# Optimization experiments

Measured on AMD Instinct MI355X. Metric: run time of the kernel, lower is better.

The kernel has to match this reference:

```python
import jax, jax.numpy as jnp
import numpy as np
from jax import lax

# Config matching init_kwargs
H, W = 64, 64
DIM = 160
HEADS = 5
KD = DIM // HEADS            # key_dim = head_dim = 32 (attn_ratio=1 -> d == key_dim)
WS = 14                       # window size -> n = 196 tokens per window
HIDDEN = int(DIM * 4.0)
EPS = 1e-5


def _make_bias_idxs(ws):
    pts = [(i, j) for i in range(ws) for j in range(ws)]
    offs, idxs = {}, []
    for p1 in pts:
        for p2 in pts:
            o = (abs(p1[0] - p2[0]), abs(p1[1] - p2[1]))
            if o not in offs:
                offs[o] = len(offs)
            idxs.append(offs[o])
    n = len(pts)
    return np.asarray(idxs, np.int32).reshape(n, n), len(offs)


def setup_inputs() -> dict:
    key = jax.random.key(0)
    ks = jax.random.split(key, 10)
    bias_idxs_np, n_off = _make_bias_idxs(WS)  # [196,196], 196 unique offsets
    s = 0.02
    return {
        "x": jax.random.normal(ks[0], (16, H * W, DIM), jnp.float32),
        "ln1_g": jnp.ones((DIM,), jnp.float32),
        "ln1_b": jnp.zeros((DIM,), jnp.float32),
        "qkv_w": jax.random.normal(ks[1], (3 * KD * HEADS, DIM), jnp.float32) * s,
        "qkv_b": jnp.zeros((3 * KD * HEADS,), jnp.float32),
        "proj_w": jax.random.normal(ks[2], (DIM, KD * HEADS), jnp.float32) * s,
        "proj_b": jnp.zeros((DIM,), jnp.float32),
        "attn_biases": jax.random.normal(ks[3], (HEADS, n_off), jnp.float32) * s,
        "conv_w": jax.random.normal(ks[4], (DIM, 1, 3, 3), jnp.float32) * s,  # depthwise OIHW
        "bn_g": jnp.ones((DIM,), jnp.float32),
        "bn_b": jnp.zeros((DIM,), jnp.float32),
        "ln2_g": jnp.ones((DIM,), jnp.float32),
        "ln2_b": jnp.zeros((DIM,), jnp.float32),
        "fc1_w": jax.random.normal(ks[5], (HIDDEN, DIM), jnp.float32) * s,
        "fc1_b": jnp.zeros((HIDDEN,), jnp.float32),
        "fc2_w": jax.random.normal(ks[6], (DIM, HIDDEN), jnp.float32) * s,
        "fc2_b": jnp.zeros((DIM,), jnp.float32),
        "bias_idxs": jnp.asarray(bias_idxs_np),
    }


def _layernorm(x, g, b):
    m = jnp.mean(x, -1, keepdims=True)
    v = jnp.mean(jnp.square(x - m), -1, keepdims=True)
    return (x - m) * lax.rsqrt(v + EPS) * g + b


def reference(x, ln1_g, ln1_b, qkv_w, qkv_b, proj_w, proj_b, attn_biases,
              conv_w, bn_g, bn_b, ln2_g, ln2_b, fc1_w, fc1_b, fc2_w, fc2_b,
              bias_idxs):
    b, l, c = x.shape
    res = x
    # ---- window partition (64 -> pad 70 -> 5x5 windows of 14x14 = 196 tokens)
    pad_b = (WS - H % WS) % WS
    pad_r = (WS - W % WS) % WS
    xg = x.reshape(b, H, W, c)
    xg = jnp.pad(xg, ((0, 0), (0, pad_b), (0, pad_r), (0, 0)))
    ph, pw = H + pad_b, W + pad_r
    nh, nw = ph // WS, pw // WS
    n = WS * WS
    xw = xg.reshape(b, nh, WS, nw, WS, c).transpose(0, 1, 3, 2, 4, 5).reshape(b * nh * nw, n, c)
    # ---- attention with gathered relative-position bias
    xn = _layernorm(xw, ln1_g, ln1_b)
    qkv = (xn @ qkv_w.T + qkv_b).reshape(xw.shape[0], n, HEADS, 3 * KD)
    q, k, v = qkv[..., :KD], qkv[..., KD:2 * KD], qkv[..., 2 * KD:]
    bias = attn_biases[:, bias_idxs]  # [HEADS, n, n]
    scores = jnp.einsum('bnhd,bmhd->bhnm', q, k) * (KD ** -0.5) + bias
    a = jax.nn.softmax(scores, axis=-1)
    out = jnp.einsum('bhnm,bmhd->bnhd', a, v).reshape(xw.shape[0], n, HEADS * KD)
    xw = out @ proj_w.T + proj_b
    # ---- window merge + unpad
    xg = xw.reshape(b, nh, nw, WS, WS, c).transpose(0, 1, 3, 2, 4, 5).reshape(b, ph, pw, c)
    xg = xg[:, :H, :W]
    x = res + xg.reshape(b, l, c)
    # ---- depthwise 3x3 conv + BN (eval: running_mean=0, running_var=1)
    xc = x.transpose(0, 2, 1).reshape(b, c, H, W)
    y = lax.conv_general_dilated(xc, conv_w, (1, 1), [(1, 1), (1, 1)],
                                 dimension_numbers=('NCHW', 'OIHW', 'NCHW'),
                                 feature_group_count=c)
    y = y * (bn_g * lax.rsqrt(jnp.float32(1.0 + EPS)))[None, :, None, None] + bn_b[None, :, None, None]
    x = y.reshape(b, c, l).transpose(0, 2, 1)
    # ---- MLP with pre-LN and exact GELU
    xn = _layernorm(x, ln2_g, ln2_b)
    h = jax.nn.gelu(xn @ fc1_w.T + fc1_b, approximate=False)
    m = h @ fc2_w.T + fc2_b
    return x + m
```

## Files before the change

kernel.cpp:

```cpp
#include <hip/hip_runtime.h>
#include <hip/hip_bf16.h>
#include <math.h>

typedef unsigned short ushort;
typedef __attribute__((ext_vector_type(4))) float f32x4;
typedef __attribute__((ext_vector_type(8))) short s16x8;
typedef __attribute__((ext_vector_type(4))) short s16x4;
typedef __attribute__((ext_vector_type(4))) ushort u16x4;

#define H_    64
#define W_    64
#define DIM   160
#define HEADS 5
#define KD    32
#define WS    14
#define NTOK  196
#define NWIN  400
#define HIDDEN 640
#define EPS   1e-5f
#define NROW  (NWIN*NTOK)
#define BATCH 16
#define L_    (H_*W_)
#define MROW  (BATCH*L_)
#define CS    0.25507875861f
#define GSTRIPS 4

#if __has_builtin(__builtin_amdgcn_exp2f)
#define EXP2(x) __builtin_amdgcn_exp2f(x)
#else
#define EXP2(x) exp2f(x)
#endif

__device__ __forceinline__ ushort f2bfbits(float f) {
    unsigned u = __float_as_uint(f);
    unsigned r = (u + 0x7fffu + ((u >> 16) & 1u)) >> 16;
    return (ushort)r;
}

__global__ __launch_bounds__(256) void pre_kernel(
    const float* __restrict__ qkv_w, const float* __restrict__ proj_w,
    const float* __restrict__ fc1_w, const float* __restrict__ fc2_w,
    const float* __restrict__ conv_w, const float* __restrict__ bn_g,
    const float* __restrict__ abias, const int* __restrict__ bidx,
    ushort* __restrict__ wb, float* __restrict__ cwT,
    float* __restrict__ biasP, int n_off)
{
    const int gid = blockIdx.x * 256 + threadIdx.x;
    if (gid < 19200) {
        float4 v = ((const float4*)qkv_w)[gid];
        u16x4 o = { f2bfbits(v.x), f2bfbits(v.y), f2bfbits(v.z), f2bfbits(v.w) };
        *(u16x4*)(wb + gid * 4) = o;
    } else if (gid < 25600) {
        const int i = gid - 19200;
        float4 v = ((const float4*)proj_w)[i];
        u16x4 o = { f2bfbits(v.x), f2bfbits(v.y), f2bfbits(v.z), f2bfbits(v.w) };
        *(u16x4*)(wb + 76800 + i * 4) = o;
    } else if (gid < 38400) {
        const int idx = gid - 25600;
        const int l = idx & 63, rest = idx >> 6;
        const int jj = rest % 5, ht = rest / 5;
        const float* src = fc1_w + (size_t)(ht * 16 + (l & 15)) * 160
                         + jj * 32 + (l >> 4) * 8;
        const float4 v0 = *(const float4*)src;
        const float4 v1 = *(const float4*)(src + 4);
        u16x4 o0 = { f2bfbits(v0.x), f2bfbits(v0.y), f2bfbits(v0.z), f2bfbits(v0.w) };
        u16x4 o1 = { f2bfbits(v1.x), f2bfbits(v1.y), f2bfbits(v1.z), f2bfbits(v1.w) };
        *(u16x4*)(wb + 102400 + idx * 8)     = o0;
        *(u16x4*)(wb + 102400 + idx * 8 + 4) = o1;
    } else if (gid < 51200) {
        const int idx = gid - 38400;
        const int l = idx & 63, f = idx >> 6;
        const int dt = f % 10, u = f / 10;
        const float* base = fc2_w + (size_t)(dt * 16 + (l & 15)) * HIDDEN
                          + u * 32 + 4 * (l >> 4);
        const float4 v0 = *(const float4*)base;
        const float4 v1 = *(const float4*)(base + 16);
        u16x4 o0 = { f2bfbits(v0.x), f2bfbits(v0.y), f2bfbits(v0.z), f2bfbits(v0.w) };
        u16x4 o1 = { f2bfbits(v1.x), f2bfbits(v1.y), f2bfbits(v1.z), f2bfbits(v1.w) };
        *(u16x4*)(wb + 204800 + idx * 8)     = o0;
        *(u16x4*)(wb + 204800 + idx * 8 + 4) = o1;
    } else if (gid < 51560) {
        const int i = gid - 51200;
        const int t = i / 40, c4 = (i % 40) * 4;
#pragma unroll
        for (int j = 0; j < 4; ++j) {
            const int c = c4 + j;
            cwT[t * DIM + c] = conv_w[c * 9 + t] * bn_g[c] * rsqrtf(1.0f + EPS);
        }
    } else if (gid < 267880) {
        const int idx = gid - 51560;
        const int ln = idx & 255, f = idx >> 8;
        const int h = f / 169, rem = f % 169;
        const int qt = rem / 13, kt = rem % 13;
        int q = qt * 16 + (ln & 15); if (q > NTOK - 1) q = NTOK - 1;
        const int k0 = kt * 16 + (ln >> 4) * 4;
        float4 o;
        float* ov = (float*)&o;
#pragma unroll
        for (int r = 0; r < 4; ++r) {
            const int k = k0 + r;
            ov[r] = (k < NTOK)
                ? abias[h * n_off + bidx[q * NTOK + k]] * 1.4426950408889634f
                : 0.f;
        }
        *(float4*)(biasP + (size_t)idx * 4) = o;
    }
}

__global__ __launch_bounds__(256) void ln1_win_kernel(
    const float* __restrict__ x, const float* __restrict__ g,
    const float* __restrict__ b, ushort* __restrict__ xn)
{
    const int row = blockIdx.x * 4 + (threadIdx.x >> 6);
    const int win = row / NTOK, tok = row % NTOK;
    const int bb = win / 25, wr = (win % 25) / 5, wc = win % 5;
    const int gh = wr * WS + tok / WS, gw = wc * WS + tok % WS;
    const bool valid = (gh < H_) && (gw < W_);
    const float* xrow = x + ((size_t)bb * L_ + (size_t)gh * W_ + gw) * DIM;
    const int lane = threadIdx.x & 63;
    float v0 = 0.f, v1 = 0.f, v2 = 0.f;
    if (valid) {
        v0 = xrow[lane];
        v1 = xrow[lane + 64];
        if (lane < 32) v2 = xrow[lane + 128];
    }
    float s  = v0 + v1 + v2;
    float sq = v0 * v0 + v1 * v1 + v2 * v2;
#pragma unroll
    for (int off = 32; off; off >>= 1) { s += __shfl_xor(s, off); sq += __shfl_xor(sq, off); }
    const float mean = s * (1.0f / DIM);
    const float var  = sq * (1.0f / DIM) - mean * mean;
    const float rs   = rsqrtf(var + EPS);
    ushort* orow = xn + (size_t)row * DIM;
    orow[lane]      = f2bfbits((v0 - mean) * rs * g[lane]      + b[lane]);
    orow[lane + 64] = f2bfbits((v1 - mean) * rs * g[lane + 64] + b[lane + 64]);
    if (lane < 32) orow[lane + 128] = f2bfbits((v2 - mean) * rs * g[lane + 128] + b[lane + 128]);
}

template <int EPI>
__global__ __launch_bounds__(512) void gemm_mfma(
    const ushort* __restrict__ A, const ushort* __restrict__ Wb,
    const float* __restrict__ bias, void* __restrict__ Cv,
    const float* __restrict__ extra, int M, int N)
{
    __shared__ ushort Bs[160][164];
    const int tid = threadIdx.x;
    const int wv = tid >> 6, ln = tid & 63;
    const int g = ln >> 4, l15 = ln & 15;
    const int wvm = wv & 3, wvn = wv >> 2;
    const int n0 = blockIdx.y * 160;
    const int strip0 = blockIdx.x * GSTRIPS;

    for (int e = tid; e < 160 * 20; e += 512) {
        const int row = e / 20, part = e % 20;
        *(int4*)&Bs[row][part * 8] =
            *(const int4*)(Wb + (size_t)(n0 + row) * 160 + part * 8);
    }

    s16x8 a[2][5];
    {
        const int m0 = strip0 * 128;
#pragma unroll
        for (int mt = 0; mt < 2; ++mt) {
            int am = m0 + wvm * 32 + mt * 16 + l15; if (am >= M) am = M - 1;
            const ushort* ap = A + (size_t)am * 160 + g * 8;
#pragma unroll
            for (int s = 0; s < 5; ++s) a[mt][s] = *(const s16x8*)(ap + s * 32);
        }
    }
    __syncthreads();

    for (int s = 0; s < GSTRIPS; ++s) {
        const int m0 = (strip0 + s) * 128;
        if (m0 >= M) break;

        f32x4 acc[2][5] = {};
#pragma unroll
        for (int j = 0; j < 5; ++j) {
#pragma unroll
            for (int nt = 0; nt < 5; ++nt) {
                const s16x8 bf = *(const s16x8*)&Bs[wvn * 80 + nt * 16 + l15][j * 32 + g * 8];
                acc[0][nt] = __builtin_amdgcn_mfma_f32_16x16x32_bf16(bf, a[0][j], acc[0][nt], 0, 0, 0);
                acc[1][nt] = __builtin_amdgcn_mfma_f32_16x16x32_bf16(bf, a[1][j], acc[1][nt], 0, 0, 0);
            }
        }

        if (s + 1 < GSTRIPS) {
            const int mn = (strip0 + s + 1) * 128;
#pragma unroll
            for (int mt = 0; mt < 2; ++mt) {
                int am = mn + wvm * 32 + mt * 16 + l15; if (am >= M) am = M - 1;
                const ushort* ap = A + (size_t)am * 160 + g * 8;
#pragma unroll
                for (int jj = 0; jj < 5; ++jj) a[mt][jj] = *(const s16x8*)(ap + jj * 32);
            }
        }

#pragma unroll
        for (int mt = 0; mt < 2; ++mt) {
            const int m = m0 + wvm * 32 + mt * 16 + l15;
            if (m >= M) continue;
            if (EPI == 0) {
                ushort* orow = (ushort*)Cv + (size_t)m * N;
#pragma unroll
                for (int nt = 0; nt < 5; ++nt) {
                    const int n = n0 + wvn * 80 + nt * 16 + g * 4;
                    const float4 bn = *(const float4*)&bias[n];
                    const float sc = ((n % 96) < 32) ? CS : 1.0f;
                    u16x4 o = { f2bfbits((acc[mt][nt][0] + bn.x) * sc),
                                f2bfbits((acc[mt][nt][1] + bn.y) * sc),
                                f2bfbits((acc[mt][nt][2] + bn.z) * sc),
                                f2bfbits((acc[mt][nt][3] + bn.w) * sc) };
                    *(u16x4*)(orow + n) = o;
                }
            } else {
                const int win = m / NTOK, tok = m % NTOK;
                const int bb = win / 25, wr = (win % 25) / 5, wc = win % 5;
                const int gh = wr * WS + tok / WS, gw = wc * WS + tok % WS;
                if (gh < H_ && gw < W_) {
                    const size_t rowoff = ((size_t)bb * L_ + (size_t)gh * W_ + gw) * DIM;
                    float* orow = (float*)Cv + rowoff;
                    const float* erow = extra + rowoff;
#pragma unroll
                    for (int nt = 0; nt < 5; ++nt) {
                        const int n = n0 + wvn * 80 + nt * 16 + g * 4;
                        const float4 bn = *(const float4*)&bias[n];
                        const float4 res = *(const float4*)&erow[n];
                        float4 o4 = { res.x + acc[mt][nt][0] + bn.x,
                                      res.y + acc[mt][nt][1] + bn.y,
                                      res.z + acc[mt][nt][2] + bn.z,
                                      res.w + acc[mt][nt][3] + bn.w };
                        *(float4*)&orow[n] = o4;
                    }
                }
            }
        }
    }
}

__global__ __launch_bounds__(256, 3) void mlp_fused(
    float* xo, const ushort* __restrict__ w1p, const ushort* __restrict__ w2p,
    const float* __restrict__ fc1_b, const float* __restrict__ fc2_b,
    const float* __restrict__ lng, const float* __restrict__ lnb)
{
    __shared__ ushort W1s[10240];
    __shared__ ushort W2s[10240];
    const int tid = threadIdx.x;
    const int wv = tid >> 6, ln = tid & 63;
    const int g = ln >> 4, l15 = ln & 15;
    const int row0 = blockIdx.x * 64 + wv * 16;

    const float* xp = xo + (size_t)(row0 + l15) * DIM + g * 8;
    float4 va[10];
    float vsum = 0.f, vsq = 0.f;
#pragma unroll
    for (int s = 0; s < 5; ++s) {
        const float4 p0 = *(const float4*)(xp + s * 32);
        const float4 p1 = *(const float4*)(xp + s * 32 + 4);
        va[s * 2] = p0; va[s * 2 + 1] = p1;
        vsum += (p0.x + p0.y) + (p0.z + p0.w) + (p1.x + p1.y) + (p1.z + p1.w);
        vsq  += (p0.x*p0.x + p0.y*p0.y) + (p0.z*p0.z + p0.w*p0.w)
              + (p1.x*p1.x + p1.y*p1.y) + (p1.z*p1.z + p1.w*p1.w);
    }
    vsum += __shfl_xor(vsum, 16); vsum += __shfl_xor(vsum, 32);
    vsq  += __shfl_xor(vsq, 16);  vsq  += __shfl_xor(vsq, 32);
    const float mean = vsum * (1.0f / DIM);
    const float rs = rsqrtf(vsq * (1.0f / DIM) - mean * mean + EPS);
    s16x8 a1[5];
#pragma unroll
    for (int s = 0; s < 5; ++s) {
        const float4 g0 = *(const float4*)(lng + s * 32 + g * 8);
        const float4 g1 = *(const float4*)(lng + s * 32 + g * 8 + 4);
        const float4 bb0 = *(const float4*)(lnb + s * 32 + g * 8);
        const float4 bb1 = *(const float4*)(lnb + s * 32 + g * 8 + 4);
        const float4 p0 = va[s * 2], p1 = va[s * 2 + 1];
        ushort o[8];
        o[0] = f2bfbits((p0.x - mean) * rs * g0.x + bb0.x);
        o[1] = f2bfbits((p0.y - mean) * rs * g0.y + bb0.y);
        o[2] = f2bfbits((p0.z - mean) * rs * g0.z + bb0.z);
        o[3] = f2bfbits((p0.w - mean) * rs * g0.w + bb0.w);
        o[4] = f2bfbits((p1.x - mean) * rs * g1.x + bb1.x);
        o[5] = f2bfbits((p1.y - mean) * rs * g1.y + bb1.y);
        o[6] = f2bfbits((p1.z - mean) * rs * g1.z + bb1.z);
        o[7] = f2bfbits((p1.w - mean) * rs * g1.w + bb1.w);
        a1[s] = *(const s16x8*)o;
    }

    f32x4 oacc[10] = {};
    for (int c = 0; c < 10; ++c) {
        if (c) __syncthreads();
        const ushort* s1 = w1p + c * 10240;
        const ushort* s2 = w2p + c * 10240;
        for (int e = tid; e < 1280; e += 256) {
            *(int4*)&W1s[e * 8] = *(const int4*)(s1 + e * 8);
            *(int4*)&W2s[e * 8] = *(const int4*)(s2 + e * 8);
        }
        __syncthreads();

#pragma unroll
        for (int p = 0; p < 2; ++p) {
            f32x4 h0 = {0.f,0.f,0.f,0.f}, h1 = {0.f,0.f,0.f,0.f};
#pragma unroll
            for (int jj = 0; jj < 5; ++jj) {
                const s16x8 wfe = *(const s16x8*)&W1s[(((p * 2) * 5 + jj) * 64 + ln) * 8];
                const s16x8 wfo = *(const s16x8*)&W1s[(((p * 2 + 1) * 5 + jj) * 64 + ln) * 8];
                h0 = __builtin_amdgcn_mfma_f32_16x16x32_bf16(wfe, a1[jj], h0, 0, 0, 0);
                h1 = __builtin_amdgcn_mfma_f32_16x16x32_bf16(wfo, a1[jj], h1, 0, 0, 0);
            }
            const int hb0 = c * 64 + p * 32 + g * 4;
            const float4 hbe = *(const float4*)(fc1_b + hb0);
            const float4 hbo = *(const float4*)(fc1_b + hb0 + 16);
            const float hbev[4] = { hbe.x, hbe.y, hbe.z, hbe.w };
            const float hbov[4] = { hbo.x, hbo.y, hbo.z, hbo.w };
            ushort pk[8];
#pragma unroll
            for (int r = 0; r < 4; ++r) {
                float v = h0[r] + hbev[r];
                float t = EXP2(-2.302259756f * fmaf(0.044715f * v * v, v, v));
                pk[r] = f2bfbits(v * __builtin_amdgcn_rcpf(1.0f + t));
                v = h1[r] + hbov[r];
                t = EXP2(-2.302259756f * fmaf(0.044715f * v * v, v, v));
                pk[4 + r] = f2bfbits(v * __builtin_amdgcn_rcpf(1.0f + t));
            }
            const s16x8 P = *(const s16x8*)pk;
#pragma unroll
            for (int dt = 0; dt < 10; ++dt) {
                const s16x8 w2f = *(const s16x8*)&W2s[((p * 10 + dt) * 64 + ln) * 8];
                oacc[dt] = __builtin_amdgcn_mfma_f32_16x16x32_bf16(P, w2f, oacc[dt], 0, 0, 0);
            }
        }
    }

#pragma unroll
    for (int dt = 0; dt < 10; ++dt) {
        const float bn = fc2_b[dt * 16 + l15];
#pragma unroll
        for (int r = 0; r < 4; ++r) {
            const size_t off = (size_t)(row0 + g * 4 + r) * DIM + dt * 16 + l15;
            xo[off] += oacc[dt][r] + bn;
        }
    }
}

__global__ __launch_bounds__(256) void attn_mfma_kernel(
    const ushort* __restrict__ qkv, const float* __restrict__ biasP,
    ushort* __restrict__ out)
{
    __shared__ ushort Ks[208][40];
    __shared__ ushort VT[32][212];
    const int win = blockIdx.x / HEADS;
    const int h   = blockIdx.x % HEADS;
    const int tid = threadIdx.x;
    const size_t base = (size_t)win * NTOK;
    const ushort* qbase = qkv + base * 480 + h * 96;

    for (int e = tid; e < 208 * 4; e += 256) {
        const int row = e >> 2, part = e & 3;
        const int gr = row < NTOK ? row : NTOK - 1;
        *(int4*)&Ks[row][part * 8] = *(const int4*)(qbase + (size_t)gr * 480 + 32 + part * 8);
    }
    for (int e = tid; e < NTOK * 4; e += 256) {
        const int key = e >> 2, part = e & 3;
        int4 p = *(const int4*)(qbase + (size_t)key * 480 + 64 + part * 8);
        const ushort* u = (const ushort*)&p;
#pragma unroll
        for (int j = 0; j < 8; ++j) VT[part * 8 + j][key] = u[j];
    }
    for (int e = tid; e < 12 * 32; e += 256) VT[e & 31][NTOK + (e >> 5)] = 0;
    __syncthreads();

    const int wv = tid >> 6, ln = tid & 63, g = ln >> 4, l15 = ln & 15;

    for (int qt = wv; qt < 13; qt += 4) {
        const int qr = qt * 16 + l15;
        const int qc = qr < NTOK ? qr : NTOK - 1;
        const s16x8 qf = *(const s16x8*)(qbase + (size_t)qc * 480 + g * 8);
        const float* bq = biasP + ((size_t)(h * 13 + qt) * 13) * 1024;

        f32x4 S[13];
#pragma unroll
        for (int kt = 0; kt < 13; ++kt)
            S[kt] = *(const f32x4*)(bq + kt * 1024 + ln * 4);
#pragma unroll
        for (int kt = 0; kt < 13; ++kt) {
            const s16x8 kf = *(const s16x8*)&Ks[kt * 16 + l15][g * 8];
            S[kt] = __builtin_amdgcn_mfma_f32_16x16x32_bf16(kf, qf, S[kt], 0, 0, 0);
        }
        float mx = -1e30f;
#pragma unroll
        for (int kt = 0; kt < 13; ++kt) {
#pragma unroll
            for (int r = 0; r < 4; ++r) {
                if (kt == 12) {
                    const int key = 192 + g * 4 + r;
                    if (key >= NTOK) S[kt][r] = -1e30f;
                }
                mx = fmaxf(mx, S[kt][r]);
            }
        }
        mx = fmaxf(mx, __shfl_xor(mx, 16));
        mx = fmaxf(mx, __shfl_xor(mx, 32));

        float sum = 0.f;
        s16x4 P[13];
#pragma unroll
        for (int kt = 0; kt < 13; ++kt) {
            const float p0 = EXP2(S[kt][0] - mx);
            const float p1 = EXP2(S[kt][1] - mx);
            const float p2 = EXP2(S[kt][2] - mx);
            const float p3 = EXP2(S[kt][3] - mx);
            sum += (p0 + p1) + (p2 + p3);
            P[kt] = (s16x4){ (short)f2bfbits(p0), (short)f2bfbits(p1),
                             (short)f2bfbits(p2), (short)f2bfbits(p3) };
        }
        sum += __shfl_xor(sum, 16);
        sum += __shfl_xor(sum, 32);

        f32x4 o0 = {0.f,0.f,0.f,0.f}, o1 = {0.f,0.f,0.f,0.f};
#pragma unroll
        for (int kt = 0; kt < 13; ++kt) {
            const s16x4 vf0 = *(const s16x4*)&VT[l15][kt * 16 + g * 4];
            const s16x4 vf1 = *(const s16x4*)&VT[16 + l15][kt * 16 + g * 4];
            o0 = __builtin_amdgcn_mfma_f32_16x16x16bf16_1k(vf0, P[kt], o0, 0, 0, 0);
            o1 = __builtin_amdgcn_mfma_f32_16x16x16bf16_1k(vf1, P[kt], o1, 0, 0, 0);
        }
        if (qr < NTOK) {
            const float inv = 1.0f / sum;
            ushort* op = out + (base + qr) * DIM + h * KD;
            u16x4 w0 = { f2bfbits(o0[0] * inv), f2bfbits(o0[1] * inv),
                         f2bfbits(o0[2] * inv), f2bfbits(o0[3] * inv) };
            u16x4 w1 = { f2bfbits(o1[0] * inv), f2bfbits(o1[1] * inv),
                         f2bfbits(o1[2] * inv), f2bfbits(o1[3] * inv) };
            *(u16x4*)(op + g * 4)      = w0;
            *(u16x4*)(op + 16 + g * 4) = w1;
        }
    }
}

__global__ __launch_bounds__(256) void dwconv_bn_kernel(
    const float* __restrict__ xin, const float* __restrict__ cwT,
    const float* __restrict__ bnb, float* __restrict__ xout)
{
    const int gid = blockIdx.x * 256 + threadIdx.x;
    const int pos = gid / 40, c4 = (gid % 40) * 4;
    const int bb = pos >> 12, hw = pos & 4095;
    const int hh = hw >> 6, ww = hw & 63;
    float4 acc = *(const float4*)&bnb[c4];
#pragma unroll
    for (int kh = -1; kh <= 1; ++kh) {
        const int ih = hh + kh;
        if (ih < 0 || ih >= H_) continue;
#pragma unroll
        for (int kw = -1; kw <= 1; ++kw) {
            const int iw = ww + kw;
            if (iw < 0 || iw >= W_) continue;
            const float4 xv = *(const float4*)&xin[((size_t)(bb << 12) + (ih << 6) + iw) * DIM + c4];
            const float4 wv = *(const float4*)&cwT[((kh + 1) * 3 + (kw + 1)) * DIM + c4];
            acc.x = fmaf(xv.x, wv.x, acc.x);
            acc.y = fmaf(xv.y, wv.y, acc.y);
            acc.z = fmaf(xv.z, wv.z, acc.z);
            acc.w = fmaf(xv.w, wv.w, acc.w);
        }
    }
    *(float4*)&xout[(size_t)pos * DIM + c4] = acc;
}

extern "C" void kernel_launch(void* const* d_in, const int* in_sizes, int n_in,
                              void* d_out, int out_size, void* d_ws, size_t ws_size,
                              hipStream_t stream)
{
    const float* x      = (const float*)d_in[0];
    const float* ln1_g  = (const float*)d_in[1];
    const float* ln1_b  = (const float*)d_in[2];
    const float* qkv_w  = (const float*)d_in[3];
    const float* qkv_b  = (const float*)d_in[4];
    const float* proj_w = (const float*)d_in[5];
    const float* proj_b = (const float*)d_in[6];
    const float* abias  = (const float*)d_in[7];
    const float* conv_w = (const float*)d_in[8];
    const float* bn_g   = (const float*)d_in[9];
    const float* bn_b   = (const float*)d_in[10];
    const float* ln2_g  = (const float*)d_in[11];
    const float* ln2_b  = (const float*)d_in[12];
    const float* fc1_w  = (const float*)d_in[13];
    const float* fc1_b  = (const float*)d_in[14];
    const float* fc2_w  = (const float*)d_in[15];
    const float* fc2_b  = (const float*)d_in[16];
    const int*   bidx   = (const int*)d_in[17];
    const int    n_off  = in_sizes[7] / HEADS;

    char* ws = (char*)d_ws;
    ushort* xn    = (ushort*)(ws);
    ushort* qkv   = (ushort*)(ws + 25088000);
    ushort* ao    = (ushort*)(ws + 100352000);
    float*  biasP = (float*)(ws + 125440000);
    float*  x1    = (float*)(ws + 125440000);
    ushort* wb    = (ushort*)(ws + 167383040);
    float*  cwT   = (float*)(ws + 167997440);
    float*  x2    = (float*)d_out;

    const int mblocks = (NROW + 128 * GSTRIPS - 1) / (128 * GSTRIPS);

    pre_kernel<<<dim3(1047), dim3(256), 0, stream>>>(
        qkv_w, proj_w, fc1_w, fc2_w, conv_w, bn_g, abias, bidx, wb, cwT, biasP, n_off);

    ln1_win_kernel<<<dim3(NROW / 4), dim3(256), 0, stream>>>(x, ln1_g, ln1_b, xn);

    gemm_mfma<0><<<dim3(mblocks, 3), dim3(512), 0, stream>>>(
        xn, wb, qkv_b, (void*)qkv, nullptr, NROW, 480);

    attn_mfma_kernel<<<dim3(NWIN * HEADS), dim3(256), 0, stream>>>(qkv, biasP, ao);

    gemm_mfma<1><<<dim3(mblocks, 1), dim3(512), 0, stream>>>(
        ao, wb + 76800, proj_b, (void*)x1, x, NROW, 160);

    dwconv_bn_kernel<<<dim3(MROW * 40 / 256), dim3(256), 0, stream>>>(
        x1, cwT, bn_b, x2);

    mlp_fused<<<dim3(MROW / 64), dim3(256), 0, stream>>>(
        x2, wb + 102400, wb + 204800, fc1_b, fc2_b, ln2_g, ln2_b);
}
```

Measured before the change: 237.1 us.

## Store attention bias table in bf16 and widen MLP blocks to 512 threads

The precomputed per-head relative-position bias table is now written as bf16 instead of fp32 and widened back to fp32 in the attention kernel. This halves the bias bytes each attention block streams from memory, at the cost of bf16 rounding of the bias. Separately, the fused MLP kernel now runs 512-thread blocks covering 128 rows, so each shared-memory weight chunk load serves twice as many rows. The launch bound asks for 4 blocks per SM, which may force register pressure or spills.

```diff
diff --git a/kernel.cpp b/kernel.cpp
--- a/kernel.cpp
+++ b/kernel.cpp
@@ -36,6 +36,9 @@
     unsigned r = (u + 0x7fffu + ((u >> 16) & 1u)) >> 16;
     return (ushort)r;
 }
+__device__ __forceinline__ float bf2f(ushort u) {
+    return __uint_as_float(((unsigned)u) << 16);
+}
 
 __global__ __launch_bounds__(256) void pre_kernel(
     const float* __restrict__ qkv_w, const float* __restrict__ proj_w,
@@ -43,7 +46,7 @@
     const float* __restrict__ conv_w, const float* __restrict__ bn_g,
     const float* __restrict__ abias, const int* __restrict__ bidx,
     ushort* __restrict__ wb, float* __restrict__ cwT,
-    float* __restrict__ biasP, int n_off)
+    ushort* __restrict__ biasPb, int n_off)
 {
     const int gid = blockIdx.x * 256 + threadIdx.x;
     if (gid < 19200) {
@@ -94,16 +97,15 @@
         const int qt = rem / 13, kt = rem % 13;
         int q = qt * 16 + (ln & 15); if (q > NTOK - 1) q = NTOK - 1;
         const int k0 = kt * 16 + (ln >> 4) * 4;
-        float4 o;
-        float* ov = (float*)&o;
+        ushort o[4];
 #pragma unroll
         for (int r = 0; r < 4; ++r) {
             const int k = k0 + r;
-            ov[r] = (k < NTOK)
-                ? abias[h * n_off + bidx[q * NTOK + k]] * 1.4426950408889634f
-                : 0.f;
-        }
-        *(float4*)(biasP + (size_t)idx * 4) = o;
+            o[r] = (k < NTOK)
+                ? f2bfbits(abias[h * n_off + bidx[q * NTOK + k]] * 1.4426950408889634f)
+                : (ushort)0;
+        }
+        *(u16x4*)(biasPb + (size_t)idx * 4) = *(const u16x4*)o;
     }
 }
 
@@ -238,7 +240,7 @@
     }
 }
 
-__global__ __launch_bounds__(256, 3) void mlp_fused(
+__global__ __launch_bounds__(512, 4) void mlp_fused(
     float* xo, const ushort* __restrict__ w1p, const ushort* __restrict__ w2p,
     const float* __restrict__ fc1_b, const float* __restrict__ fc2_b,
     const float* __restrict__ lng, const float* __restrict__ lnb)
@@ -248,7 +250,7 @@
     const int tid = threadIdx.x;
     const int wv = tid >> 6, ln = tid & 63;
     const int g = ln >> 4, l15 = ln & 15;
-    const int row0 = blockIdx.x * 64 + wv * 16;
+    const int row0 = blockIdx.x * 128 + wv * 16;
 
     const float* xp = xo + (size_t)(row0 + l15) * DIM + g * 8;
     float4 va[10];
@@ -291,7 +293,7 @@
         if (c) __syncthreads();
         const ushort* s1 = w1p + c * 10240;
         const ushort* s2 = w2p + c * 10240;
-        for (int e = tid; e < 1280; e += 256) {
+        for (int e = tid; e < 1280; e += 512) {
             *(int4*)&W1s[e * 8] = *(const int4*)(s1 + e * 8);
             *(int4*)&W2s[e * 8] = *(const int4*)(s2 + e * 8);
         }
@@ -343,7 +345,7 @@
 }
 
 __global__ __launch_bounds__(256) void attn_mfma_kernel(
-    const ushort* __restrict__ qkv, const float* __restrict__ biasP,
+    const ushort* __restrict__ qkv, const ushort* __restrict__ biasPb,
     ushort* __restrict__ out)
 {
     __shared__ ushort Ks[208][40];
@@ -375,12 +377,14 @@
         const int qr = qt * 16 + l15;
         const int qc = qr < NTOK ? qr : NTOK - 1;
         const s16x8 qf = *(const s16x8*)(qbase + (size_t)qc * 480 + g * 8);
-        const float* bq = biasP + ((size_t)(h * 13 + qt) * 13) * 1024;
+        const ushort* bq = biasPb + ((size_t)(h * 13 + qt) * 13) * 1024;
 
         f32x4 S[13];
 #pragma unroll
-        for (int kt = 0; kt < 13; ++kt)
-            S[kt] = *(const f32x4*)(bq + kt * 1024 + ln * 4);
+        for (int kt = 0; kt < 13; ++kt) {
+            const u16x4 bv = *(const u16x4*)(bq + kt * 1024 + ln * 4);
+            S[kt] = (f32x4){ bf2f(bv[0]), bf2f(bv[1]), bf2f(bv[2]), bf2f(bv[3]) };
+        }
 #pragma unroll
         for (int kt = 0; kt < 13; ++kt) {
             const s16x8 kf = *(const s16x8*)&Ks[kt * 16 + l15][g * 8];
@@ -490,26 +494,26 @@
     const int    n_off  = in_sizes[7] / HEADS;
 
     char* ws = (char*)d_ws;
-    ushort* xn    = (ushort*)(ws);
-    ushort* qkv   = (ushort*)(ws + 25088000);
-    ushort* ao    = (ushort*)(ws + 100352000);
-    float*  biasP = (float*)(ws + 125440000);
-    float*  x1    = (float*)(ws + 125440000);
-    ushort* wb    = (ushort*)(ws + 167383040);
-    float*  cwT   = (float*)(ws + 167997440);
-    float*  x2    = (float*)d_out;
+    ushort* xn     = (ushort*)(ws);
+    ushort* qkv    = (ushort*)(ws + 25088000);
+    ushort* ao     = (ushort*)(ws + 100352000);
+    ushort* biasPb = (ushort*)(ws + 125440000);
+    float*  x1     = (float*)(ws + 125440000);
+    ushort* wb     = (ushort*)(ws + 167383040);
+    float*  cwT    = (float*)(ws + 167997440);
+    float*  x2     = (float*)d_out;
 
     const int mblocks = (NROW + 128 * GSTRIPS - 1) / (128 * GSTRIPS);
 
     pre_kernel<<<dim3(1047), dim3(256), 0, stream>>>(
-        qkv_w, proj_w, fc1_w, fc2_w, conv_w, bn_g, abias, bidx, wb, cwT, biasP, n_off);
+        qkv_w, proj_w, fc1_w, fc2_w, conv_w, bn_g, abias, bidx, wb, cwT, biasPb, n_off);
 
     ln1_win_kernel<<<dim3(NROW / 4), dim3(256), 0, stream>>>(x, ln1_g, ln1_b, xn);
 
     gemm_mfma<0><<<dim3(mblocks, 3), dim3(512), 0, stream>>>(
         xn, wb, qkv_b, (void*)qkv, nullptr, NROW, 480);
 
-    attn_mfma_kernel<<<dim3(NWIN * HEADS), dim3(256), 0, stream>>>(qkv, biasP, ao);
+    attn_mfma_kernel<<<dim3(NWIN * HEADS), dim3(256), 0, stream>>>(qkv, biasPb, ao);
 
     gemm_mfma<1><<<dim3(mblocks, 1), dim3(512), 0, stream>>>(
         ao, wb + 76800, proj_b, (void*)x1, x, NROW, 160);
@@ -517,6 +521,6 @@
     dwconv_bn_kernel<<<dim3(MROW * 40 / 256), dim3(256), 0, stream>>>(
         x1, cwT, bn_b, x2);
 
-    mlp_fused<<<dim3(MROW / 64), dim3(256), 0, stream>>>(
+    mlp_fused<<<dim3(MROW / 128), dim3(512), 0, stream>>>(
         x2, wb + 102400, wb + 204800, fc1_b, fc2_b, ln2_g, ln2_b);
 }
```

Measured after the change: 240.0 us. About the same (+1.2%).
